# Kernel tuning notes

Hardware: AMD Instinct MI355X
Metric: run time of the kernel (lower is better)

The kernel has to match this reference:

```python
import jax, jax.numpy as jnp
import numpy as np

N_HEADS = 16
D_EMBED = 1024
D_HEAD = D_EMBED // N_HEADS  # 64
B, L = 8, 4096


def setup_inputs() -> dict:
    key = jax.random.key(0)
    ks = jax.random.split(key, 8)
    s = 1.0 / np.sqrt(D_EMBED)  # linear-layer-ish init scale
    x = jax.random.normal(ks[0], (B, L, D_EMBED), dtype=jnp.float32)
    mask = jnp.ones((B, L), dtype=bool)
    Wq = jax.random.normal(ks[1], (D_EMBED, D_EMBED), dtype=jnp.float32) * s
    bq = jnp.zeros((D_EMBED,), dtype=jnp.float32)
    Wk = jax.random.normal(ks[2], (D_EMBED, D_EMBED), dtype=jnp.float32) * s
    bk = jnp.zeros((D_EMBED,), dtype=jnp.float32)
    Wv = jax.random.normal(ks[3], (D_EMBED, N_HEADS), dtype=jnp.float32) * s
    bv = jnp.zeros((N_HEADS,), dtype=jnp.float32)
    return {"x": x, "mask": mask, "Wq": Wq, "bq": bq, "Wk": Wk, "bk": bk, "Wv": Wv, "bv": bv}


def reference(x, mask, Wq, bq, Wk, bk, Wv, bv):
    # Projections. q,k: [B, H, L, Dh]; v: [B, H, L] (value head-dim is 1).
    q = (x @ Wq + bq).reshape(B, L, N_HEADS, D_HEAD).transpose(0, 2, 1, 3)
    k = (x @ Wk + bk).reshape(B, L, N_HEADS, D_HEAD).transpose(0, 2, 1, 3)
    v = (x @ Wv + bv).transpose(0, 2, 1)  # [B, H, L]
    # scores @ value == Q @ (K^T V) / sqrt(Dh) by linearity (value head-dim 1),
    # so the L x L score matrix is never materialized.
    ktv = jnp.einsum("bhld,bhl->bhd", k, v)               # [B, H, Dh]
    z = jnp.einsum("bhld,bhd->bhl", q, ktv) / np.sqrt(D_HEAD)  # [B, H, L]
    # GumbelSigmoid in deterministic (eval) mode: plain sigmoid of the logits.
    p_attn = jax.nn.sigmoid(z)
    # masked_fill(~mask.unsqueeze(1), 0.0); dropout is identity in eval mode.
    p_attn = jnp.where(mask[:, None, :], p_attn, 0.0)
    return p_attn
```

## Files before the change

kernel.cpp:

```cpp
#include <hip/hip_runtime.h>
#include <hip/hip_bf16.h>
#include <math.h>

#define BATCH 8
#define LTOT 4096
#define DEMB 1024
#define NH 16
#define DH 64

#define CHUNKS 32
#define ROWS_PER_BLOCK (LTOT / CHUNKS)
#define TILE 64
#define NTILES (ROWS_PER_BLOCK / TILE)

#define WS_S     0
#define WS_SV    131072
#define WS_WQ    131200
#define WS_C     262272
#define WS_SPART 262400
#define WS_NEED  ((size_t)(WS_SPART + BATCH * CHUNKS * DEMB * NH) * 4)

__device__ __forceinline__ float dot_row_lds(const float* __restrict__ xrow,
                                             const float* __restrict__ w, int h) {
  float a0 = 0.f, a1 = 0.f, a2 = 0.f, a3 = 0.f;
  #pragma unroll 4
  for (int i = 0; i < DEMB; i += 16) {
    const float4 p0 = *(const float4*)&xrow[i + 0];
    const float4 p1 = *(const float4*)&xrow[i + 4];
    const float4 p2 = *(const float4*)&xrow[i + 8];
    const float4 p3 = *(const float4*)&xrow[i + 12];
    a0 += p0.x * w[(i + 0) * NH + h] + p0.y * w[(i + 1) * NH + h]
        + p0.z * w[(i + 2) * NH + h] + p0.w * w[(i + 3) * NH + h];
    a1 += p1.x * w[(i + 4) * NH + h] + p1.y * w[(i + 5) * NH + h]
        + p1.z * w[(i + 6) * NH + h] + p1.w * w[(i + 7) * NH + h];
    a2 += p2.x * w[(i + 8) * NH + h] + p2.y * w[(i + 9) * NH + h]
        + p2.z * w[(i + 10) * NH + h] + p2.w * w[(i + 11) * NH + h];
    a3 += p3.x * w[(i + 12) * NH + h] + p3.y * w[(i + 13) * NH + h]
        + p3.z * w[(i + 14) * NH + h] + p3.w * w[(i + 15) * NH + h];
  }
  return (a0 + a1) + (a2 + a3);
}

__global__ __launch_bounds__(1024) void k1_fused(
    const float* __restrict__ x, const float* __restrict__ Wv,
    const float* __restrict__ bv, float* __restrict__ Spart,
    float* __restrict__ S, float* __restrict__ sv, int direct) {
  __shared__ float wv_lds[DEMB * NH];
  __shared__ float vt[2][TILE * NH];
  __shared__ float sv_red[1024];

  const int b = blockIdx.x >> 5;
  const int chunk = blockIdx.x & 31;
  const int l0 = chunk * ROWS_PER_BLOCK;
  const int t = threadIdx.x;

  #pragma unroll
  for (int j = t * 4; j < DEMB * NH; j += 1024 * 4)
    *(float4*)&wv_lds[j] = *(const float4*)&Wv[j];
  __syncthreads();

  const int r = t >> 4;
  const int h = t & 15;
  const float bvh = bv[h];
  const float* xb = x + (size_t)b * LTOT * DEMB;

  float acc[16];
  #pragma unroll
  for (int hh = 0; hh < 16; ++hh) acc[hh] = 0.f;
  float sv_acc = 0.f;

  {
    const float v = bvh + dot_row_lds(xb + (size_t)(l0 + r) * DEMB, wv_lds, h);
    vt[0][r * NH + h] = v;
    sv_acc += v;
  }

  for (int tile = 0; tile < NTILES; ++tile) {
    __syncthreads();
    if (tile + 1 < NTILES) {
      const float v = bvh +
          dot_row_lds(xb + (size_t)(l0 + (tile + 1) * TILE + r) * DEMB, wv_lds, h);
      vt[(tile + 1) & 1][r * NH + h] = v;
      sv_acc += v;
    }
    const float* vbuf = vt[tile & 1];
    const int lbase = l0 + tile * TILE;
    #pragma unroll 4
    for (int l = 0; l < TILE; ++l) {
      const float xv = xb[(size_t)(lbase + l) * DEMB + t];
      const float4 v0 = *(const float4*)&vbuf[l * NH + 0];
      const float4 v1 = *(const float4*)&vbuf[l * NH + 4];
      const float4 v2 = *(const float4*)&vbuf[l * NH + 8];
      const float4 v3 = *(const float4*)&vbuf[l * NH + 12];
      acc[0] += xv * v0.x;  acc[1] += xv * v0.y;  acc[2] += xv * v0.z;  acc[3] += xv * v0.w;
      acc[4] += xv * v1.x;  acc[5] += xv * v1.y;  acc[6] += xv * v1.z;  acc[7] += xv * v1.w;
      acc[8] += xv * v2.x;  acc[9] += xv * v2.y;  acc[10] += xv * v2.z; acc[11] += xv * v2.w;
      acc[12] += xv * v3.x; acc[13] += xv * v3.y; acc[14] += xv * v3.z; acc[15] += xv * v3.w;
    }
  }

  if (direct) {
    float* dst = Spart + ((size_t)blockIdx.x << 14) + t * NH;
    *(float4*)&dst[0]  = make_float4(acc[0], acc[1], acc[2], acc[3]);
    *(float4*)&dst[4]  = make_float4(acc[4], acc[5], acc[6], acc[7]);
    *(float4*)&dst[8]  = make_float4(acc[8], acc[9], acc[10], acc[11]);
    *(float4*)&dst[12] = make_float4(acc[12], acc[13], acc[14], acc[15]);
  } else {
    float* Sb = S + ((size_t)b << 14);
    #pragma unroll
    for (int hh = 0; hh < 16; ++hh) atomicAdd(&Sb[t * NH + hh], acc[hh]);
  }

  sv_red[t] = sv_acc;
  __syncthreads();
  if (t < 16) {
    float s = 0.f;
    #pragma unroll
    for (int rr = 0; rr < 64; ++rr) s += sv_red[rr * 16 + t];
    atomicAdd(&sv[b * NH + t], s);
  }
}

__global__ __launch_bounds__(256) void k1b_reduce(
    const float* __restrict__ Spart, float* __restrict__ S) {
  const int b = blockIdx.x >> 4;
  const int seg = blockIdx.x & 15;
  #pragma unroll
  for (int k = 0; k < 4; ++k) {
    const int idx = seg * 1024 + k * 256 + threadIdx.x;
    float s = 0.f;
    #pragma unroll 8
    for (int c = 0; c < CHUNKS; ++c)
      s += Spart[((size_t)(b * CHUNKS + c) << 14) + idx];
    S[((size_t)b << 14) + idx] = s;
  }
}

__global__ __launch_bounds__(1024) void k2_ktv_wq(
    const float* __restrict__ Wq, const float* __restrict__ bq,
    const float* __restrict__ Wk, const float* __restrict__ bk,
    const float* __restrict__ S, const float* __restrict__ sv,
    float* __restrict__ wq_eff, float* __restrict__ cvec) {
  __shared__ float part[16][DH];
  __shared__ float ktv[DH];
  const int b = blockIdx.x >> 4;
  const int h = blockIdx.x & 15;
  const int t = threadIdx.x;
  const float* Sb = S + ((size_t)b << 14);

  const int d = t & 63, seg = t >> 6;
  float p = 0.f;
  #pragma unroll 4
  for (int i = seg * 64; i < seg * 64 + 64; ++i)
    p += Wk[(size_t)i * DEMB + h * DH + d] * Sb[i * NH + h];
  part[seg][d] = p;
  __syncthreads();
  if (t < 64) {
    float s = 0.f;
    #pragma unroll
    for (int k = 0; k < 16; ++k) s += part[k][t];
    s += bk[h * DH + t] * sv[b * NH + h];
    ktv[t] = s;
  }
  __syncthreads();

  {
    const int i = t;
    const float* wrow = &Wq[(size_t)i * DEMB + h * DH];
    float s0 = 0.f, s1 = 0.f;
    #pragma unroll
    for (int dd = 0; dd < DH; dd += 8) {
      const float4 w4 = *(const float4*)&wrow[dd];
      const float4 w5 = *(const float4*)&wrow[dd + 4];
      s0 += w4.x * ktv[dd] + w4.y * ktv[dd + 1] + w4.z * ktv[dd + 2] + w4.w * ktv[dd + 3];
      s1 += w5.x * ktv[dd + 4] + w5.y * ktv[dd + 5] + w5.z * ktv[dd + 6] + w5.w * ktv[dd + 7];
    }
    wq_eff[((size_t)b << 14) + i * NH + h] = s0 + s1;
  }
  if (t == 0) {
    float s = 0.f;
    for (int dd = 0; dd < DH; ++dd) s += bq[h * DH + dd] * ktv[dd];
    cvec[b * NH + h] = s;
  }
}

__global__ __launch_bounds__(1024) void k3_z_sigmoid(
    const float* __restrict__ x, const int* __restrict__ mask,
    const float* __restrict__ wq_eff, const float* __restrict__ cvec,
    float* __restrict__ out) {
  __shared__ float wq_lds[DEMB * NH];
  __shared__ float c_lds[NH];

  const int b = blockIdx.x >> 5;
  const int chunk = blockIdx.x & 31;
  const int l0 = chunk * ROWS_PER_BLOCK;
  const int t = threadIdx.x;

  const float* wq_b = wq_eff + ((size_t)b << 14);
  #pragma unroll
  for (int j = t * 4; j < DEMB * NH; j += 1024 * 4)
    *(float4*)&wq_lds[j] = *(const float4*)&wq_b[j];
  if (t < 16) c_lds[t] = cvec[b * NH + t];
  __syncthreads();

  const int r = t >> 4;
  const int h = t & 15;
  const float c = c_lds[h];
  const float* xb = x + (size_t)b * LTOT * DEMB;

  #pragma unroll
  for (int tile = 0; tile < NTILES; ++tile) {
    const int l = l0 + tile * TILE + r;
    float z = c + dot_row_lds(xb + (size_t)l * DEMB, wq_lds, h);
    z *= 0.125f;
    float pr = 1.f / (1.f + __expf(-z));
    if (mask[b * LTOT + l] == 0) pr = 0.f;
    out[((size_t)(b * NH + h)) * LTOT + l] = pr;
  }
}

extern "C" void kernel_launch(void* const* d_in, const int* in_sizes, int n_in,
                              void* d_out, int out_size, void* d_ws, size_t ws_size,
                              hipStream_t stream) {
  const float* x  = (const float*)d_in[0];
  const int* mask = (const int*)d_in[1];
  const float* Wq = (const float*)d_in[2];
  const float* bq = (const float*)d_in[3];
  const float* Wk = (const float*)d_in[4];
  const float* bk = (const float*)d_in[5];
  const float* Wv = (const float*)d_in[6];
  const float* bv = (const float*)d_in[7];
  float* out = (float*)d_out;
  float* ws = (float*)d_ws;

  float* S      = ws + WS_S;
  float* sv     = ws + WS_SV;
  float* wq_eff = ws + WS_WQ;
  float* cvec   = ws + WS_C;
  float* Spart  = ws + WS_SPART;

  const int direct = (ws_size >= WS_NEED) ? 1 : 0;

  hipMemsetAsync(sv, 0, 128 * sizeof(float), stream);
  if (!direct) hipMemsetAsync(S, 0, (size_t)BATCH * DEMB * NH * sizeof(float), stream);

  k1_fused<<<dim3(BATCH * CHUNKS), dim3(1024), 0, stream>>>(x, Wv, bv, Spart, S, sv, direct);
  if (direct)
    k1b_reduce<<<dim3(BATCH * 16), dim3(256), 0, stream>>>(Spart, S);
  k2_ktv_wq<<<dim3(BATCH * NH), dim3(1024), 0, stream>>>(Wq, bq, Wk, bk, S, sv, wq_eff, cvec);
  k3_z_sigmoid<<<dim3(BATCH * CHUNKS), dim3(1024), 0, stream>>>(x, mask, wq_eff, cvec, out);
}
```

Before: 380.5 us.

## Use XOR-swizzled head-major weight layout and two-rows-per-thread projections

Stores Wv and the effective Wq weights in LDS head-major with an XOR swizzle on float4 groups. Each thread reads its weights as float4s and computes two rows per pass, so every weight load feeds two rows, and the strided scalar LDS reads with bank conflicts go away. The previous double-buffered tile pipeline in k1 becomes one projection phase followed by an outer-product phase that uses float4 x loads and 4x4 register tiles. It also adds an occupancy launch-bound hint and doubles the reduce kernel's grid. In exchange, every thread reads two x rows with a stride, which could raise register use and change cache behaviour.

```diff
diff --git a/kernel.cpp b/kernel.cpp
--- a/kernel.cpp
+++ b/kernel.cpp
@@ -7,112 +7,103 @@
 #define DEMB 1024
 #define NH 16
 #define DH 64
-
 #define CHUNKS 32
-#define ROWS_PER_BLOCK (LTOT / CHUNKS)
-#define TILE 64
-#define NTILES (ROWS_PER_BLOCK / TILE)
+#define RPB 128
 
 #define WS_S     0
-#define WS_SV    131072
-#define WS_WQ    131200
-#define WS_C     262272
-#define WS_SPART 262400
-#define WS_NEED  ((size_t)(WS_SPART + BATCH * CHUNKS * DEMB * NH) * 4)
-
-__device__ __forceinline__ float dot_row_lds(const float* __restrict__ xrow,
-                                             const float* __restrict__ w, int h) {
-  float a0 = 0.f, a1 = 0.f, a2 = 0.f, a3 = 0.f;
-  #pragma unroll 4
-  for (int i = 0; i < DEMB; i += 16) {
-    const float4 p0 = *(const float4*)&xrow[i + 0];
-    const float4 p1 = *(const float4*)&xrow[i + 4];
-    const float4 p2 = *(const float4*)&xrow[i + 8];
-    const float4 p3 = *(const float4*)&xrow[i + 12];
-    a0 += p0.x * w[(i + 0) * NH + h] + p0.y * w[(i + 1) * NH + h]
-        + p0.z * w[(i + 2) * NH + h] + p0.w * w[(i + 3) * NH + h];
-    a1 += p1.x * w[(i + 4) * NH + h] + p1.y * w[(i + 5) * NH + h]
-        + p1.z * w[(i + 6) * NH + h] + p1.w * w[(i + 7) * NH + h];
-    a2 += p2.x * w[(i + 8) * NH + h] + p2.y * w[(i + 9) * NH + h]
-        + p2.z * w[(i + 10) * NH + h] + p2.w * w[(i + 11) * NH + h];
-    a3 += p3.x * w[(i + 12) * NH + h] + p3.y * w[(i + 13) * NH + h]
-        + p3.z * w[(i + 14) * NH + h] + p3.w * w[(i + 15) * NH + h];
-  }
-  return (a0 + a1) + (a2 + a3);
-}
-
-__global__ __launch_bounds__(1024) void k1_fused(
+#define WS_SV    (WS_S + BATCH*DEMB*NH)
+#define WS_WQ    (WS_SV + BATCH*NH)
+#define WS_C     (WS_WQ + BATCH*DEMB*NH)
+#define WS_SPART (WS_C + BATCH*NH)
+#define WS_NEED  ((size_t)(WS_SPART + (size_t)BATCH*CHUNKS*DEMB*NH) * 4)
+
+
+__global__ __launch_bounds__(1024, 8) void k1_fused(
     const float* __restrict__ x, const float* __restrict__ Wv,
     const float* __restrict__ bv, float* __restrict__ Spart,
     float* __restrict__ S, float* __restrict__ sv, int direct) {
-  __shared__ float wv_lds[DEMB * NH];
-  __shared__ float vt[2][TILE * NH];
+  __shared__ float wv_sw[DEMB * NH];
+  __shared__ float vt[RPB * NH];
   __shared__ float sv_red[1024];
 
   const int b = blockIdx.x >> 5;
   const int chunk = blockIdx.x & 31;
-  const int l0 = chunk * ROWS_PER_BLOCK;
+  const int l0 = chunk * RPB;
   const int t = threadIdx.x;
 
-  #pragma unroll
-  for (int j = t * 4; j < DEMB * NH; j += 1024 * 4)
-    *(float4*)&wv_lds[j] = *(const float4*)&Wv[j];
-  __syncthreads();
-
-  const int r = t >> 4;
-  const int h = t & 15;
-  const float bvh = bv[h];
-  const float* xb = x + (size_t)b * LTOT * DEMB;
-
-  float acc[16];
-  #pragma unroll
-  for (int hh = 0; hh < 16; ++hh) acc[hh] = 0.f;
-  float sv_acc = 0.f;
-
-  {
-    const float v = bvh + dot_row_lds(xb + (size_t)(l0 + r) * DEMB, wv_lds, h);
-    vt[0][r * NH + h] = v;
-    sv_acc += v;
-  }
-
-  for (int tile = 0; tile < NTILES; ++tile) {
-    __syncthreads();
-    if (tile + 1 < NTILES) {
-      const float v = bvh +
-          dot_row_lds(xb + (size_t)(l0 + (tile + 1) * TILE + r) * DEMB, wv_lds, h);
-      vt[(tile + 1) & 1][r * NH + h] = v;
-      sv_acc += v;
-    }
-    const float* vbuf = vt[tile & 1];
-    const int lbase = l0 + tile * TILE;
+  {
+    const float4* wrow = (const float4*)&Wv[(size_t)t * NH];
+    const float4 r0 = wrow[0], r1 = wrow[1], r2 = wrow[2], r3 = wrow[3];
+    const float vals[16] = {r0.x, r0.y, r0.z, r0.w, r1.x, r1.y, r1.z, r1.w,
+                            r2.x, r2.y, r2.z, r2.w, r3.x, r3.y, r3.z, r3.w};
+    const int g = t >> 2, lo = t & 3;
+    #pragma unroll
+    for (int h = 0; h < 16; ++h)
+      wv_sw[h * DEMB + (((g ^ h) << 2) + lo)] = vals[h];
+  }
+  __syncthreads();
+
+  {
+    const int h = t & 15;
+    const int rp = t >> 4;
+    const float4* x40 = (const float4*)(x + ((size_t)b * LTOT + l0 + 2 * rp) * DEMB);
+    const float4* x41 = x40 + 256;
+    const float4* wv4 = (const float4*)&wv_sw[h * DEMB];
+    float c00 = 0.f, c01 = 0.f, c10 = 0.f, c11 = 0.f;
     #pragma unroll 4
-    for (int l = 0; l < TILE; ++l) {
-      const float xv = xb[(size_t)(lbase + l) * DEMB + t];
-      const float4 v0 = *(const float4*)&vbuf[l * NH + 0];
-      const float4 v1 = *(const float4*)&vbuf[l * NH + 4];
-      const float4 v2 = *(const float4*)&vbuf[l * NH + 8];
-      const float4 v3 = *(const float4*)&vbuf[l * NH + 12];
-      acc[0] += xv * v0.x;  acc[1] += xv * v0.y;  acc[2] += xv * v0.z;  acc[3] += xv * v0.w;
-      acc[4] += xv * v1.x;  acc[5] += xv * v1.y;  acc[6] += xv * v1.z;  acc[7] += xv * v1.w;
-      acc[8] += xv * v2.x;  acc[9] += xv * v2.y;  acc[10] += xv * v2.z; acc[11] += xv * v2.w;
-      acc[12] += xv * v3.x; acc[13] += xv * v3.y; acc[14] += xv * v3.z; acc[15] += xv * v3.w;
-    }
-  }
-
-  if (direct) {
-    float* dst = Spart + ((size_t)blockIdx.x << 14) + t * NH;
-    *(float4*)&dst[0]  = make_float4(acc[0], acc[1], acc[2], acc[3]);
-    *(float4*)&dst[4]  = make_float4(acc[4], acc[5], acc[6], acc[7]);
-    *(float4*)&dst[8]  = make_float4(acc[8], acc[9], acc[10], acc[11]);
-    *(float4*)&dst[12] = make_float4(acc[12], acc[13], acc[14], acc[15]);
-  } else {
-    float* Sb = S + ((size_t)b << 14);
-    #pragma unroll
-    for (int hh = 0; hh < 16; ++hh) atomicAdd(&Sb[t * NH + hh], acc[hh]);
-  }
-
-  sv_red[t] = sv_acc;
-  __syncthreads();
+    for (int g = 0; g < 256; ++g) {
+      const float4 w = wv4[g ^ h];
+      const float4 a = x40[g];
+      const float4 d = x41[g];
+      c00 += a.x * w.x + a.y * w.y;
+      c01 += a.z * w.z + a.w * w.w;
+      c10 += d.x * w.x + d.y * w.y;
+      c11 += d.z * w.z + d.w * w.w;
+    }
+    const float bvh = bv[h];
+    const float v0 = bvh + c00 + c01;
+    const float v1 = bvh + c10 + c11;
+    vt[(2 * rp) * NH + h] = v0;
+    vt[(2 * rp + 1) * NH + h] = v1;
+    sv_red[t] = v0 + v1;
+  }
+  __syncthreads();
+
+  {
+    const int hg = t & 3;
+    const int i4 = t >> 2;
+    const float4* xb4 = (const float4*)(x + ((size_t)b * LTOT + l0) * DEMB);
+    const float4* vt4 = (const float4*)vt;
+    float4 accA = {0, 0, 0, 0}, accB = accA, accC = accA, accD = accA;
+    #pragma unroll 4
+    for (int l = 0; l < RPB; ++l) {
+      const float4 xv = xb4[l * 256 + i4];
+      const float4 vv = vt4[l * 4 + hg];
+      accA.x += xv.x * vv.x; accA.y += xv.x * vv.y; accA.z += xv.x * vv.z; accA.w += xv.x * vv.w;
+      accB.x += xv.y * vv.x; accB.y += xv.y * vv.y; accB.z += xv.y * vv.z; accB.w += xv.y * vv.w;
+      accC.x += xv.z * vv.x; accC.y += xv.z * vv.y; accC.z += xv.z * vv.z; accC.w += xv.z * vv.w;
+      accD.x += xv.w * vv.x; accD.y += xv.w * vv.y; accD.z += xv.w * vv.z; accD.w += xv.w * vv.w;
+    }
+    const int col0 = i4 << 2;
+    if (direct) {
+      float* dst = Spart + ((size_t)blockIdx.x << 14);
+      *(float4*)&dst[(col0 + 0) * NH + hg * 4] = accA;
+      *(float4*)&dst[(col0 + 1) * NH + hg * 4] = accB;
+      *(float4*)&dst[(col0 + 2) * NH + hg * 4] = accC;
+      *(float4*)&dst[(col0 + 3) * NH + hg * 4] = accD;
+    } else {
+      float* Sb = S + ((size_t)b << 14);
+      const float4 av[4] = {accA, accB, accC, accD};
+      #pragma unroll
+      for (int c = 0; c < 4; ++c) {
+        atomicAdd(&Sb[(col0 + c) * NH + hg * 4 + 0], av[c].x);
+        atomicAdd(&Sb[(col0 + c) * NH + hg * 4 + 1], av[c].y);
+        atomicAdd(&Sb[(col0 + c) * NH + hg * 4 + 2], av[c].z);
+        atomicAdd(&Sb[(col0 + c) * NH + hg * 4 + 3], av[c].w);
+      }
+    }
+  }
+
   if (t < 16) {
     float s = 0.f;
     #pragma unroll
@@ -123,11 +114,11 @@
 
 __global__ __launch_bounds__(256) void k1b_reduce(
     const float* __restrict__ Spart, float* __restrict__ S) {
-  const int b = blockIdx.x >> 4;
-  const int seg = blockIdx.x & 15;
+  const int b = blockIdx.x >> 5;
+  const int seg = blockIdx.x & 31;
   #pragma unroll
-  for (int k = 0; k < 4; ++k) {
-    const int idx = seg * 1024 + k * 256 + threadIdx.x;
+  for (int k = 0; k < 2; ++k) {
+    const int idx = seg * 512 + k * 256 + threadIdx.x;
     float s = 0.f;
     #pragma unroll 8
     for (int c = 0; c < CHUNKS; ++c)
@@ -140,7 +131,7 @@
     const float* __restrict__ Wq, const float* __restrict__ bq,
     const float* __restrict__ Wk, const float* __restrict__ bk,
     const float* __restrict__ S, const float* __restrict__ sv,
-    float* __restrict__ wq_eff, float* __restrict__ cvec) {
+    float* __restrict__ wq_sw, float* __restrict__ cvec) {
   __shared__ float part[16][DH];
   __shared__ float ktv[DH];
   const int b = blockIdx.x >> 4;
@@ -175,7 +166,7 @@
       s0 += w4.x * ktv[dd] + w4.y * ktv[dd + 1] + w4.z * ktv[dd + 2] + w4.w * ktv[dd + 3];
       s1 += w5.x * ktv[dd + 4] + w5.y * ktv[dd + 5] + w5.z * ktv[dd + 6] + w5.w * ktv[dd + 7];
     }
-    wq_eff[((size_t)b << 14) + i * NH + h] = s0 + s1;
+    wq_sw[(size_t)b * DEMB * NH + h * DEMB + ((((i >> 2) ^ h) << 2) + (i & 3))] = s0 + s1;
   }
   if (t == 0) {
     float s = 0.f;
@@ -184,39 +175,52 @@
   }
 }
 
-__global__ __launch_bounds__(1024) void k3_z_sigmoid(
+__global__ __launch_bounds__(1024, 8) void k3_z_sigmoid(
     const float* __restrict__ x, const int* __restrict__ mask,
-    const float* __restrict__ wq_eff, const float* __restrict__ cvec,
+    const float* __restrict__ wq_sw_g, const float* __restrict__ cvec,
     float* __restrict__ out) {
-  __shared__ float wq_lds[DEMB * NH];
+  __shared__ float wq_sw[DEMB * NH];
   __shared__ float c_lds[NH];
 
   const int b = blockIdx.x >> 5;
   const int chunk = blockIdx.x & 31;
-  const int l0 = chunk * ROWS_PER_BLOCK;
+  const int l0 = chunk * RPB;
   const int t = threadIdx.x;
 
-  const float* wq_b = wq_eff + ((size_t)b << 14);
+  const float4* src = (const float4*)(wq_sw_g + (size_t)b * DEMB * NH);
+  float4* dst = (float4*)wq_sw;
   #pragma unroll
-  for (int j = t * 4; j < DEMB * NH; j += 1024 * 4)
-    *(float4*)&wq_lds[j] = *(const float4*)&wq_b[j];
+  for (int j = t; j < DEMB * NH / 4; j += 1024) dst[j] = src[j];
   if (t < 16) c_lds[t] = cvec[b * NH + t];
   __syncthreads();
 
-  const int r = t >> 4;
   const int h = t & 15;
-  const float c = c_lds[h];
-  const float* xb = x + (size_t)b * LTOT * DEMB;
-
-  #pragma unroll
-  for (int tile = 0; tile < NTILES; ++tile) {
-    const int l = l0 + tile * TILE + r;
-    float z = c + dot_row_lds(xb + (size_t)l * DEMB, wq_lds, h);
-    z *= 0.125f;
-    float pr = 1.f / (1.f + __expf(-z));
-    if (mask[b * LTOT + l] == 0) pr = 0.f;
-    out[((size_t)(b * NH + h)) * LTOT + l] = pr;
-  }
+  const int rp = t >> 4;
+  const int l = l0 + 2 * rp;
+  const float4* x40 = (const float4*)(x + ((size_t)b * LTOT + l) * DEMB);
+  const float4* x41 = x40 + 256;
+  const float4* wq4 = (const float4*)&wq_sw[h * DEMB];
+  float c00 = 0.f, c01 = 0.f, c10 = 0.f, c11 = 0.f;
+  #pragma unroll 4
+  for (int g = 0; g < 256; ++g) {
+    const float4 w = wq4[g ^ h];
+    const float4 a = x40[g];
+    const float4 d = x41[g];
+    c00 += a.x * w.x + a.y * w.y;
+    c01 += a.z * w.z + a.w * w.w;
+    c10 += d.x * w.x + d.y * w.y;
+    c11 += d.z * w.z + d.w * w.w;
+  }
+  const float cb = c_lds[h];
+  const float z0 = (cb + c00 + c01) * 0.125f;
+  const float z1 = (cb + c10 + c11) * 0.125f;
+  float p0 = 1.f / (1.f + __expf(-z0));
+  float p1 = 1.f / (1.f + __expf(-z1));
+  if (mask[b * LTOT + l] == 0) p0 = 0.f;
+  if (mask[b * LTOT + l + 1] == 0) p1 = 0.f;
+  float* orow = out + ((size_t)(b * NH + h)) * LTOT;
+  orow[l] = p0;
+  orow[l + 1] = p1;
 }
 
 extern "C" void kernel_launch(void* const* d_in, const int* in_sizes, int n_in,
@@ -235,18 +239,18 @@
 
   float* S      = ws + WS_S;
   float* sv     = ws + WS_SV;
-  float* wq_eff = ws + WS_WQ;
+  float* wq_sw  = ws + WS_WQ;
   float* cvec   = ws + WS_C;
   float* Spart  = ws + WS_SPART;
 
   const int direct = (ws_size >= WS_NEED) ? 1 : 0;
 
-  hipMemsetAsync(sv, 0, 128 * sizeof(float), stream);
+  hipMemsetAsync(sv, 0, BATCH * NH * sizeof(float), stream);
   if (!direct) hipMemsetAsync(S, 0, (size_t)BATCH * DEMB * NH * sizeof(float), stream);
 
   k1_fused<<<dim3(BATCH * CHUNKS), dim3(1024), 0, stream>>>(x, Wv, bv, Spart, S, sv, direct);
   if (direct)
-    k1b_reduce<<<dim3(BATCH * 16), dim3(256), 0, stream>>>(Spart, S);
-  k2_ktv_wq<<<dim3(BATCH * NH), dim3(1024), 0, stream>>>(Wq, bq, Wk, bk, S, sv, wq_eff, cvec);
-  k3_z_sigmoid<<<dim3(BATCH * CHUNKS), dim3(1024), 0, stream>>>(x, mask, wq_eff, cvec, out);
-}
+    k1b_reduce<<<dim3(BATCH * CHUNKS), dim3(256), 0, stream>>>(Spart, S);
+  k2_ktv_wq<<<dim3(BATCH * NH), dim3(1024), 0, stream>>>(Wq, bq, Wk, bk, S, sv, wq_sw, cvec);
+  k3_z_sigmoid<<<dim3(BATCH * CHUNKS), dim3(1024), 0, stream>>>(x, mask, wq_sw, cvec, out);
+}
```

New measurement: 384.3 us. About the same (+1.0%).
